# Kernel tuning notes

Hardware: AMD Instinct MI355X
Metric: run time of the kernel (lower is better)

Reference implementation:

```python
import jax, jax.numpy as jnp
import numpy as np

B, S, E = 8, 4096, 128

def _prelu(x, a):
    return jnp.where(x >= 0, x, a * x)

def setup_inputs() -> dict:
    key = jax.random.key(0)
    ks = jax.random.split(key, 7)
    lim = 1.0 / np.sqrt(E)
    x = jax.random.normal(ks[0], (B, S, E), dtype=jnp.float32)
    Wq = jax.random.uniform(ks[1], (E, E), jnp.float32, -lim, lim)
    Wk = jax.random.uniform(ks[2], (E, E), jnp.float32, -lim, lim)
    Wv = jax.random.uniform(ks[3], (E, E), jnp.float32, -lim, lim)
    bq = jax.random.uniform(ks[4], (E,), jnp.float32, -lim, lim)
    bk = jax.random.uniform(ks[5], (E,), jnp.float32, -lim, lim)
    bv = jax.random.uniform(ks[6], (E,), jnp.float32, -lim, lim)
    # PReLU default: single shared slope initialized to 0.25
    aq = jnp.array(0.25, dtype=jnp.float32)
    ak = jnp.array(0.25, dtype=jnp.float32)
    av = jnp.array(0.25, dtype=jnp.float32)
    return {"x": x, "Wq": Wq, "bq": bq, "aq": aq,
            "Wk": Wk, "bk": bk, "ak": ak,
            "Wv": Wv, "bv": bv, "av": av}

def reference(x, Wq, bq, aq, Wk, bk, ak, Wv, bv, av):
    # Linear (y = x @ W.T + b) followed by PReLU, per nn.Sequential(Linear, PReLU)
    qx = _prelu(jnp.einsum('bse,fe->bsf', x, Wq) + bq, aq)  # [B,S,E]
    kx = _prelu(jnp.einsum('bse,fe->bsf', x, Wk) + bk, ak)
    vx = _prelu(jnp.einsum('bse,fe->bsf', x, Wv) + bv, av)
    scale = 1.0 / jnp.sqrt(jnp.asarray(E, dtype=x.dtype))
    qk = jnp.einsum('bqe,bke->bqk', qx, kx) * scale  # [B,S,S]
    attn = jax.nn.softmax(qk, axis=2)
    return jnp.einsum('bqk,bke->bqe', attn, vx)  # [B,S,E]
```

## Files before the change

### kernel.cpp

```cpp
#include <hip/hip_runtime.h>
#include <hip/hip_bf16.h>
#include <stdint.h>

typedef __bf16 bf16x8 __attribute__((ext_vector_type(8)));
typedef float f32x4 __attribute__((ext_vector_type(4)));
typedef float f32x16 __attribute__((ext_vector_type(16)));
typedef unsigned int u32x4 __attribute__((ext_vector_type(4)));

static constexpr int Bn = 8, Sn = 4096, En = 128;

__device__ __forceinline__ unsigned short f2bf(float f) {
  unsigned u = __builtin_bit_cast(unsigned, f);
  u += 0x7fffu + ((u >> 16) & 1u);
  return (unsigned short)(u >> 16);
}

__device__ __forceinline__ float bf2f(unsigned short s) {
  return __builtin_bit_cast(float, (unsigned)s << 16);
}

__device__ __forceinline__ unsigned cvtpk(float a, float b) {
  unsigned r;
  asm("v_cvt_pk_bf16_f32 %0, %1, %2" : "=v"(r) : "v"(a), "v"(b));
  return r;
}

__device__ __forceinline__ void plswap(unsigned &a, unsigned &b) {
  asm("v_permlane32_swap_b32 %0, %1" : "+v"(a), "+v"(b));
}

__global__ __launch_bounds__(256) void wconv_kernel(
    const float* __restrict__ Wq, const float* __restrict__ Wk,
    const float* __restrict__ Wv, unsigned short* __restrict__ wb)
{
  const int f4 = blockIdx.x * 256 + threadIdx.x;
  const int mat = f4 >> 12, off = f4 & 4095;
  const float* src = (mat == 0) ? Wq : (mat == 1) ? Wk : Wv;
  const float4 v = *(const float4*)&src[off * 4];
  ushort4 pk;
  pk.x = f2bf(v.x); pk.y = f2bf(v.y); pk.z = f2bf(v.z); pk.w = f2bf(v.w);
  *(ushort4*)&wb[(size_t)mat * 16384 + off * 4] = pk;
}

__global__ __launch_bounds__(512) void qkv_kernel(
    const float* __restrict__ x, const unsigned short* __restrict__ wb,
    const float* __restrict__ bq, const float* __restrict__ aq,
    const float* __restrict__ bk, const float* __restrict__ ak,
    const float* __restrict__ bv, const float* __restrict__ av,
    unsigned short* __restrict__ qo, unsigned short* __restrict__ kf,
    unsigned short* __restrict__ vf)
{
  __shared__ __align__(16) unsigned short xs[128 * 136];
  __shared__ __align__(16) unsigned short wsh[128 * 136];
  const int tid = threadIdx.x;
  const int r0 = blockIdx.x * 128;

  for (int i = 0; i < 8; ++i) {
    int cid = tid + i * 512;
    int row = cid >> 5, c4 = cid & 31;
    const float4 v = *(const float4*)&x[(size_t)(r0 + row) * 128 + c4 * 4];
    unsigned short* d = &xs[row * 136 + c4 * 4];
    d[0] = f2bf(v.x); d[1] = f2bf(v.y); d[2] = f2bf(v.z); d[3] = f2bf(v.w);
  }

  const int lane = tid & 63, wid = tid >> 6;
  const int g = lane >> 4, ln = lane & 15;
  const float* Bs[3] = {bq, bk, bv};
  const float* As[3] = {aq, ak, av};
  bf16x8 afrag[4];

  for (int mat = 0; mat < 3; ++mat) {
    __syncthreads();
    for (int i = 0; i < 4; ++i) {
      int cid = tid + i * 512;
      int row = cid >> 4, c8 = cid & 15;
      *(uint4*)&wsh[row * 136 + c8 * 8] =
          *(const uint4*)&wb[(size_t)mat * 16384 + row * 128 + c8 * 8];
    }
    __syncthreads();

    if (mat == 0) {
      for (int ks = 0; ks < 4; ++ks)
        afrag[ks] = *(const bf16x8*)&xs[(wid * 16 + ln) * 136 + ks * 32 + g * 8];
    }
    const float alpha = As[mat][0];
    f32x4 acc[8];
    for (int nt = 0; nt < 8; ++nt) acc[nt] = (f32x4)(0.f);
    for (int nt = 0; nt < 8; ++nt)
      for (int ks = 0; ks < 4; ++ks) {
        bf16x8 bfrag = *(const bf16x8*)&wsh[(nt * 16 + ln) * 136 + ks * 32 + g * 8];
        acc[nt] = __builtin_amdgcn_mfma_f32_16x16x32_bf16(afrag[ks], bfrag, acc[nt], 0, 0, 0);
      }
    const int mbase = r0 + wid * 16 + g * 4;
    for (int nt = 0; nt < 8; ++nt) {
      const int n = nt * 16 + ln;
      const float bias = Bs[mat][n];
      float vv[4];
      for (int r = 0; r < 4; ++r) {
        float t = acc[nt][r] + bias;
        vv[r] = t >= 0.f ? t : alpha * t;
      }
      if (mat == 0) {
        for (int r = 0; r < 4; ++r) qo[(size_t)(mbase + r) * 128 + n] = f2bf(vv[r]);
      } else if (mat == 1) {
        for (int r = 0; r < 4; ++r) {
          const int key = mbase + r, bb = key >> 12, sl = key & 4095;
          const size_t addr = ((size_t)bb << 20) + (size_t)(sl >> 5) * 8192
                            + nt * 1024 + ((ln >> 3) & 1) * 512
                            + (sl & 31) * 16 + ((ln & 7) << 1);
          *(unsigned short*)((char*)kf + addr) = f2bf(vv[r]);
        }
      } else {
        const int bb = mbase >> 12, sl = mbase & 4095;
        const int kb64 = sl >> 6, kk = sl & 63;
        const int ks2 = kk >> 4, hi2 = (kk >> 3) & 1, j0 = kk & 7;
        const size_t addr = ((size_t)bb << 20) + (size_t)kb64 * 16384
                          + (n >> 5) * 4096 + ks2 * 1024 + hi2 * 512
                          + (n & 31) * 16 + (j0 << 1);
        ushort4 pk;
        pk.x = f2bf(vv[0]); pk.y = f2bf(vv[1]); pk.z = f2bf(vv[2]); pk.w = f2bf(vv[3]);
        *(ushort4*)((char*)vf + addr) = pk;
      }
    }
  }
}

__device__ __forceinline__ void load_frag(const char* kfb, const char* vfb, int kt,
                                          int tid, uint4* kr, uint4* vr) {
  const char* ks = kfb + (size_t)kt * 16384;
  const char* vs = vfb + (size_t)kt * 16384;
  kr[0] = *(const uint4*)(ks + tid * 16);
  kr[1] = *(const uint4*)(ks + 8192 + tid * 16);
  vr[0] = *(const uint4*)(vs + tid * 16);
  vr[1] = *(const uint4*)(vs + 8192 + tid * 16);
}

__device__ __forceinline__ void store_frag(char* slot, int tid,
                                           const uint4* kr, const uint4* vr) {
  *(uint4*)(slot + tid * 16) = kr[0];
  *(uint4*)(slot + 8192 + tid * 16) = kr[1];
  *(uint4*)(slot + 16384 + tid * 16) = vr[0];
  *(uint4*)(slot + 24576 + tid * 16) = vr[1];
}

template <int KSPLIT>
__global__ __launch_bounds__(512, 2) void attn_kernel(
    const unsigned short* __restrict__ q,
    const unsigned short* __restrict__ kf,
    const unsigned short* __restrict__ vf,
    unsigned short* __restrict__ opart, float* __restrict__ mpart,
    float* __restrict__ lpart, float* __restrict__ out)
{
  __shared__ __align__(16) char smem[98304];
  const int tid = threadIdx.x;
  const int lane = tid & 63, wid = tid >> 6;
  const int NS = 8 * KSPLIT;
  const int bid = blockIdx.x;
  const int s_ = bid % NS;
  const int qt = bid / NS;
  const int b  = s_ / KSPLIT;
  const int kh = s_ % KSPLIT;
  const int hi = lane >> 5, ln = lane & 31;
  const size_t bOff = (size_t)b * Sn * En;

  const int nkt = (Sn / KSPLIT) / 64;
  const int kbase = kh * (Sn / KSPLIT);
  const char* kfb = (const char*)kf + ((size_t)b << 20) + (size_t)(kbase >> 5) * 8192;
  const char* vfb = (const char*)vf + ((size_t)b << 20) + (size_t)(kbase >> 6) * 16384;

  const int qrow = qt * 256 + wid * 32 + ln;
  bf16x8 qf[8];
  #pragma unroll
  for (int s = 0; s < 8; ++s)
    qf[s] = *(const bf16x8*)((const char*)(q + bOff) + (size_t)qrow * 256 + s * 32 + hi * 16);

  f32x16 acc[4];
  #pragma unroll
  for (int et = 0; et < 4; ++et) acc[et] = (f32x16)(0.f);
  float m_run = -1e30f, lsum = 0.f;

  const float cst = 1.4426950408889634f * 0.08838834764831845f;

  auto qk = [&](const char* slot, f32x16& st0, f32x16& st1) {
    const char* kp = slot + hi * 512 + ln * 16;
    st0 = (f32x16)(0.f); st1 = (f32x16)(0.f);
    __builtin_amdgcn_s_setprio(1);
    #pragma unroll
    for (int s = 0; s < 8; ++s) {
      bf16x8 kf0 = *(const bf16x8*)(kp + s * 1024);
      bf16x8 kf1 = *(const bf16x8*)(kp + 8192 + s * 1024);
      st0 = __builtin_amdgcn_mfma_f32_32x32x16_bf16(kf0, qf[s], st0, 0, 0, 0);
      st1 = __builtin_amdgcn_mfma_f32_32x32x16_bf16(kf1, qf[s], st1, 0, 0, 0);
    }
    __builtin_amdgcn_s_setprio(0);
  };

  auto sm_pv = [&](const char* slot, const f32x16& st0, const f32x16& st1) {
    const char* vp = slot + 16384 + hi * 512 + ln * 16;
    float t16[16];
    #pragma unroll
    for (int i = 0; i < 16; ++i) t16[i] = fmaxf(st0[i], st1[i]);
    float t8[8];
    #pragma unroll
    for (int i = 0; i < 8; ++i) t8[i] = fmaxf(t16[i], t16[i + 8]);
    float t4[4];
    #pragma unroll
    for (int i = 0; i < 4; ++i) t4[i] = fmaxf(t8[i], t8[i + 4]);
    float vtile = fmaxf(fmaxf(t4[0], t4[1]), fmaxf(t4[2], t4[3])) * cst;
    vtile = fmaxf(vtile, __shfl_xor(vtile, 32));

    if (__any(vtile > m_run + 8.0f)) {
      float mnew = fmaxf(m_run, vtile);
      float al = __builtin_amdgcn_exp2f(m_run - mnew);
      #pragma unroll
      for (int et = 0; et < 4; ++et) acc[et] *= al;
      lsum *= al;
      m_run = mnew;
    }

    float p[32];
    #pragma unroll
    for (int i = 0; i < 16; ++i) p[i]      = __builtin_amdgcn_exp2f(fmaf(st0[i], cst, -m_run));
    #pragma unroll
    for (int i = 0; i < 16; ++i) p[16 + i] = __builtin_amdgcn_exp2f(fmaf(st1[i], cst, -m_run));

    float s16[16];
    #pragma unroll
    for (int i = 0; i < 16; ++i) s16[i] = p[i] + p[16 + i];
    float s8[8];
    #pragma unroll
    for (int i = 0; i < 8; ++i) s8[i] = s16[i] + s16[i + 8];
    float s4[4];
    #pragma unroll
    for (int i = 0; i < 4; ++i) s4[i] = s8[i] + s8[i + 4];
    float tsum = (s4[0] + s4[1]) + (s4[2] + s4[3]);
    tsum += __shfl_xor(tsum, 32);
    lsum += tsum;

    unsigned wa[8], wb2[8];
    #pragma unroll
    for (int g2 = 0; g2 < 8; ++g2) {
      wa[g2]  = cvtpk(p[4 * g2], p[4 * g2 + 1]);
      wb2[g2] = cvtpk(p[4 * g2 + 2], p[4 * g2 + 3]);
    }
    bf16x8 pb[4];
    #pragma unroll
    for (int ks = 0; ks < 4; ++ks) {
      unsigned w0 = wa[2 * ks], w2 = wa[2 * ks + 1];
      plswap(w0, w2);
      unsigned w1 = wb2[2 * ks], w3 = wb2[2 * ks + 1];
      plswap(w1, w3);
      u32x4 w = {w0, w1, w2, w3};
      pb[ks] = __builtin_bit_cast(bf16x8, w);
    }

    __builtin_amdgcn_s_setprio(1);
    #pragma unroll
    for (int ks = 0; ks < 4; ++ks) {
      #pragma unroll
      for (int et = 0; et < 4; ++et) {
        bf16x8 vfr = *(const bf16x8*)(vp + et * 4096 + ks * 1024);
        acc[et] = __builtin_amdgcn_mfma_f32_32x32x16_bf16(vfr, pb[ks], acc[et], 0, 0, 0);
      }
    }
    __builtin_amdgcn_s_setprio(0);
  };

  char* s0 = smem;
  char* s1 = smem + 32768;
  char* s2 = smem + 65536;

  uint4 kregA[2], vregA[2], kregB[2], vregB[2];
  load_frag(kfb, vfb, 0, tid, kregA, vregA);
  store_frag(s0, tid, kregA, vregA);
  load_frag(kfb, vfb, 1, tid, kregB, vregB);
  store_frag(s1, tid, kregB, vregB);
  if (nkt > 2) load_frag(kfb, vfb, 2, tid, kregA, vregA);
  __syncthreads();
  f32x16 sA0, sA1, sB0, sB1;
  qk(s0, sA0, sA1);

  for (int t = 0; t < nkt; t += 2) {
    if (t + 2 < nkt) store_frag(s2, tid, kregA, vregA);
    if (t + 3 < nkt) load_frag(kfb, vfb, t + 3, tid, kregB, vregB);
    qk(s1, sB0, sB1);
    sm_pv(s0, sA0, sA1);
    __syncthreads();

    if (t + 3 < nkt) store_frag(s0, tid, kregB, vregB);
    if (t + 4 < nkt) load_frag(kfb, vfb, t + 4, tid, kregA, vregA);
    if (t + 2 < nkt) qk(s2, sA0, sA1);
    sm_pv(s1, sB0, sB1);
    __syncthreads();

    char* tt = s0; s0 = s2; s2 = s1; s1 = tt;
  }

  if (KSPLIT > 1 && lane < 32) {
    const size_t idx = (size_t)kh * (Bn * Sn) + (size_t)b * Sn + qt * 256 + wid * 32 + ln;
    mpart[idx] = m_run;
    lpart[idx] = lsum;
  }

  __syncthreads();
  const float inv = (KSPLIT == 1) ? (1.0f / lsum) : 1.0f;
  char* sl = smem + wid * 8192;
  char* outb;
  if (KSPLIT == 1)
    outb = (char*)(out + ((size_t)b * Sn + qt * 256 + wid * 32) * En);
  else
    outb = (char*)(opart + ((size_t)kh * (Bn * Sn) + (size_t)b * Sn + qt * 256 + wid * 32) * En);

  #pragma unroll
  for (int h = 0; h < 2; ++h) {
    #pragma unroll
    for (int e2 = 0; e2 < 2; ++e2) {
      const int et = 2 * h + e2;
      #pragma unroll
      for (int rg = 0; rg < 4; ++rg) {
        f32x4 v;
        #pragma unroll
        for (int j = 0; j < 4; ++j) v[j] = acc[et][rg * 4 + j] * inv;
        const int addr = ln * 256 + e2 * 128 + rg * 32 + hi * 16;
        *(f32x4*)(sl + (addr ^ ((ln & 7) << 4))) = v;
      }
    }
    asm volatile("s_waitcnt lgkmcnt(0)" ::: "memory");
    __builtin_amdgcn_sched_barrier(0);
    #pragma unroll
    for (int i = 0; i < 8; ++i) {
      const int flat = i * 1024 + lane * 16;
      const int qr = flat >> 8, col = flat & 255;
      f32x4 v = *(const f32x4*)(sl + ((qr * 256 + col) ^ ((qr & 7) << 4)));
      if (KSPLIT == 1) {
        *(f32x4*)(outb + (size_t)qr * 512 + h * 256 + col) = v;
      } else {
        ushort4 pk;
        pk.x = f2bf(v[0]); pk.y = f2bf(v[1]); pk.z = f2bf(v[2]); pk.w = f2bf(v[3]);
        *(ushort4*)(outb + (size_t)qr * 256 + h * 128 + (col >> 1)) = pk;
      }
    }
    if (h == 0) {
      asm volatile("s_waitcnt lgkmcnt(0)" ::: "memory");
      __builtin_amdgcn_sched_barrier(0);
    }
  }
}

template <int NSPLIT>
__global__ __launch_bounds__(256) void combine_kernel(
    const unsigned short* __restrict__ op, const float* __restrict__ mp,
    const float* __restrict__ lp, float* __restrict__ out)
{
  const int idx = blockIdx.x * 256 + threadIdx.x;
  const int row = idx >> 5;
  const int BS = Bn * Sn;
  float m = -1e30f;
  #pragma unroll
  for (int j = 0; j < NSPLIT; ++j) m = fmaxf(m, mp[j * BS + row]);
  float den = 0.f;
  f32x4 sum = (f32x4)(0.f);
  #pragma unroll
  for (int j = 0; j < NSPLIT; ++j) {
    const float w = __builtin_amdgcn_exp2f(mp[j * BS + row] - m);
    den += w * lp[j * BS + row];
    ushort4 u = *(const ushort4*)(op + (size_t)j * ((size_t)BS * En) + (size_t)idx * 4);
    f32x4 o;
    o[0] = bf2f(u.x); o[1] = bf2f(u.y); o[2] = bf2f(u.z); o[3] = bf2f(u.w);
    sum += o * w;
  }
  const float inv = 1.f / den;
  ((f32x4*)out)[idx] = sum * inv;
}

extern "C" void kernel_launch(void* const* d_in, const int* in_sizes, int n_in,
                              void* d_out, int out_size, void* d_ws, size_t ws_size,
                              hipStream_t stream) {
  const float* x  = (const float*)d_in[0];
  const float* Wq = (const float*)d_in[1];
  const float* bq = (const float*)d_in[2];
  const float* aq = (const float*)d_in[3];
  const float* Wk = (const float*)d_in[4];
  const float* bk = (const float*)d_in[5];
  const float* ak = (const float*)d_in[6];
  const float* Wv = (const float*)d_in[7];
  const float* bv = (const float*)d_in[8];
  const float* av = (const float*)d_in[9];

  const size_t BSE = (size_t)Bn * Sn * En;
  const size_t BS  = (size_t)Bn * Sn;
  char* base = (char*)d_ws;
  unsigned short* qws = (unsigned short*)base;
  unsigned short* kws = qws + BSE;
  unsigned short* vws = kws + BSE;
  const size_t fixed = 3 * BSE * 2;
  unsigned short* opart = (unsigned short*)(base + fixed);

  auto need = [&](int j) {
    return fixed + (size_t)j * BSE * 2 + (size_t)j * BS * 8 + 98304;
  };
  int split = 1;
  if (ws_size >= need(2)) split = 2;

  float* mpart = (float*)(base + fixed + (size_t)split * BSE * 2);
  float* lpart = mpart + (size_t)split * BS;
  unsigned short* wb = (unsigned short*)(lpart + (size_t)split * BS);

  wconv_kernel<<<48, 256, 0, stream>>>(Wq, Wk, Wv, wb);
  qkv_kernel<<<256, 512, 0, stream>>>(x, wb, bq, aq, bk, ak, bv, av,
                                      qws, kws, vws);
  if (split == 2) {
    attn_kernel<2><<<256, 512, 0, stream>>>(qws, kws, vws, opart, mpart, lpart,
                                            (float*)d_out);
    combine_kernel<2><<<4096, 256, 0, stream>>>(opart, mpart, lpart, (float*)d_out);
  } else {
    attn_kernel<1><<<128, 512, 0, stream>>>(qws, kws, vws, opart, mpart, lpart,
                                            (float*)d_out);
  }
}
```

Baseline: 134.8 us.

## Add 4-way key-split attention kernel with XCC-aware ticket scheduling

Adds an attention kernel that splits the key dimension four ways and launches 512 blocks instead of 256, writing bf16 partial outputs plus per-row max and sum that a 4-way combine kernel merges. Each block claims a ticket through an atomic on a per-XCC counter, so the tiles sharing a batch's K/V are placed on the same XCD to improve L2 reuse. The aim is more parallelism and occupancy (launch bounds 512,4) on the mi355x. The cost is extra partial-output traffic, a memset, a heavier combine pass, and more workspace.

```diff
diff --git a/kernel.cpp b/kernel.cpp
--- a/kernel.cpp
+++ b/kernel.cpp
@@ -347,6 +347,197 @@
   }
 }
 
+__global__ __launch_bounds__(512, 4) void attn4_kernel(
+    const unsigned short* __restrict__ q,
+    const unsigned short* __restrict__ kf,
+    const unsigned short* __restrict__ vf,
+    unsigned short* __restrict__ opart, float* __restrict__ mpart,
+    float* __restrict__ lpart, unsigned* __restrict__ tickets)
+{
+  __shared__ __align__(16) char smem[65536];
+  __shared__ int tk_sh;
+  const int tid = threadIdx.x;
+  const int lane = tid & 63, wid = tid >> 6;
+  const int hi = lane >> 5, ln = lane & 31;
+
+  if (tid == 0) {
+    unsigned xcc;
+    asm volatile("s_getreg_b32 %0, hwreg(HW_REG_XCC_ID)" : "=s"(xcc));
+    xcc &= 7u;
+    int t = -1;
+    for (int i = 0; i < 8; ++i) {
+      unsigned qx2 = (xcc + (unsigned)i) & 7u;
+      unsigned old = atomicAdd(&tickets[qx2], 1u);
+      if (old < 64u) { t = (int)(qx2 * 64u + old); break; }
+    }
+    tk_sh = t;
+  }
+  __syncthreads();
+  const int tk = tk_sh;
+  const int qx = tk >> 6, idx = tk & 63;
+  const int s_ = qx + 8 * (idx & 3);
+  const int qt = idx >> 2;
+  const int b = s_ >> 2, kh = s_ & 3;
+
+  const size_t bOff = (size_t)b * Sn * En;
+  const int nkt = 16;
+  const int kbase = kh * 1024;
+  const char* kfb = (const char*)kf + ((size_t)b << 20) + (size_t)(kbase >> 5) * 8192;
+  const char* vfb = (const char*)vf + ((size_t)b << 20) + (size_t)(kbase >> 6) * 16384;
+
+  const int qrow = qt * 256 + wid * 32 + ln;
+  bf16x8 qf[8];
+  #pragma unroll
+  for (int s = 0; s < 8; ++s)
+    qf[s] = *(const bf16x8*)((const char*)(q + bOff) + (size_t)qrow * 256 + s * 32 + hi * 16);
+
+  f32x16 acc[4];
+  #pragma unroll
+  for (int et = 0; et < 4; ++et) acc[et] = (f32x16)(0.f);
+  float m_run = -1e30f, lsum = 0.f;
+  const float cst = 1.4426950408889634f * 0.08838834764831845f;
+
+  char* const s0 = smem;
+  char* const s1 = smem + 32768;
+
+  uint4 kreg[2], vreg[2];
+  load_frag(kfb, vfb, 0, tid, kreg, vreg);
+  store_frag(s0, tid, kreg, vreg);
+  load_frag(kfb, vfb, 1, tid, kreg, vreg);
+  __syncthreads();
+
+  for (int kt = 0; kt < nkt; ++kt) {
+    const char* cur = (kt & 1) ? s1 : s0;
+    const char* kp = cur + hi * 512 + ln * 16;
+    const char* vp = cur + 16384 + hi * 512 + ln * 16;
+
+    f32x16 st0 = (f32x16)(0.f), st1 = (f32x16)(0.f);
+    __builtin_amdgcn_s_setprio(1);
+    #pragma unroll
+    for (int s = 0; s < 8; ++s) {
+      bf16x8 kf0 = *(const bf16x8*)(kp + s * 1024);
+      bf16x8 kf1 = *(const bf16x8*)(kp + 8192 + s * 1024);
+      st0 = __builtin_amdgcn_mfma_f32_32x32x16_bf16(kf0, qf[s], st0, 0, 0, 0);
+      st1 = __builtin_amdgcn_mfma_f32_32x32x16_bf16(kf1, qf[s], st1, 0, 0, 0);
+    }
+    __builtin_amdgcn_s_setprio(0);
+
+    float t16[16];
+    #pragma unroll
+    for (int i = 0; i < 16; ++i) t16[i] = fmaxf(st0[i], st1[i]);
+    float t8[8];
+    #pragma unroll
+    for (int i = 0; i < 8; ++i) t8[i] = fmaxf(t16[i], t16[i + 8]);
+    float t4[4];
+    #pragma unroll
+    for (int i = 0; i < 4; ++i) t4[i] = fmaxf(t8[i], t8[i + 4]);
+    float vtile = fmaxf(fmaxf(t4[0], t4[1]), fmaxf(t4[2], t4[3])) * cst;
+    vtile = fmaxf(vtile, __shfl_xor(vtile, 32));
+
+    if (__any(vtile > m_run + 8.0f)) {
+      float mnew = fmaxf(m_run, vtile);
+      float al = __builtin_amdgcn_exp2f(m_run - mnew);
+      #pragma unroll
+      for (int et = 0; et < 4; ++et) acc[et] *= al;
+      lsum *= al;
+      m_run = mnew;
+    }
+
+    float p[32];
+    #pragma unroll
+    for (int i = 0; i < 16; ++i) p[i]      = __builtin_amdgcn_exp2f(fmaf(st0[i], cst, -m_run));
+    #pragma unroll
+    for (int i = 0; i < 16; ++i) p[16 + i] = __builtin_amdgcn_exp2f(fmaf(st1[i], cst, -m_run));
+
+    float s16[16];
+    #pragma unroll
+    for (int i = 0; i < 16; ++i) s16[i] = p[i] + p[16 + i];
+    float s8[8];
+    #pragma unroll
+    for (int i = 0; i < 8; ++i) s8[i] = s16[i] + s16[i + 8];
+    float s4[4];
+    #pragma unroll
+    for (int i = 0; i < 4; ++i) s4[i] = s8[i] + s8[i + 4];
+    float tsum = (s4[0] + s4[1]) + (s4[2] + s4[3]);
+    tsum += __shfl_xor(tsum, 32);
+    lsum += tsum;
+
+    unsigned wa[8], wb2[8];
+    #pragma unroll
+    for (int g2 = 0; g2 < 8; ++g2) {
+      wa[g2]  = cvtpk(p[4 * g2], p[4 * g2 + 1]);
+      wb2[g2] = cvtpk(p[4 * g2 + 2], p[4 * g2 + 3]);
+    }
+    bf16x8 pb[4];
+    #pragma unroll
+    for (int ks = 0; ks < 4; ++ks) {
+      unsigned w0 = wa[2 * ks], w2 = wa[2 * ks + 1];
+      plswap(w0, w2);
+      unsigned w1 = wb2[2 * ks], w3 = wb2[2 * ks + 1];
+      plswap(w1, w3);
+      u32x4 w = {w0, w1, w2, w3};
+      pb[ks] = __builtin_bit_cast(bf16x8, w);
+    }
+
+    __builtin_amdgcn_s_setprio(1);
+    #pragma unroll
+    for (int ks = 0; ks < 4; ++ks) {
+      #pragma unroll
+      for (int et = 0; et < 4; ++et) {
+        bf16x8 vfr = *(const bf16x8*)(vp + et * 4096 + ks * 1024);
+        acc[et] = __builtin_amdgcn_mfma_f32_32x32x16_bf16(vfr, pb[ks], acc[et], 0, 0, 0);
+      }
+    }
+    __builtin_amdgcn_s_setprio(0);
+
+    __syncthreads();
+    if (kt + 1 < nkt) store_frag((kt & 1) ? s0 : s1, tid, kreg, vreg);
+    __syncthreads();
+    if (kt + 2 < nkt) load_frag(kfb, vfb, kt + 2, tid, kreg, vreg);
+  }
+
+  if (lane < 32) {
+    const size_t idx2 = (size_t)kh * (Bn * Sn) + (size_t)b * Sn + qt * 256 + wid * 32 + ln;
+    mpart[idx2] = m_run;
+    lpart[idx2] = lsum;
+  }
+
+  __syncthreads();
+  char* sl = smem + wid * 8192;
+  char* outb = (char*)(opart + ((size_t)kh * (Bn * Sn) + (size_t)b * Sn + qt * 256 + wid * 32) * En);
+
+  #pragma unroll
+  for (int h = 0; h < 2; ++h) {
+    #pragma unroll
+    for (int e2 = 0; e2 < 2; ++e2) {
+      const int et = 2 * h + e2;
+      #pragma unroll
+      for (int rg = 0; rg < 4; ++rg) {
+        f32x4 v;
+        #pragma unroll
+        for (int j = 0; j < 4; ++j) v[j] = acc[et][rg * 4 + j];
+        const int addr = ln * 256 + e2 * 128 + rg * 32 + hi * 16;
+        *(f32x4*)(sl + (addr ^ ((ln & 7) << 4))) = v;
+      }
+    }
+    asm volatile("s_waitcnt lgkmcnt(0)" ::: "memory");
+    __builtin_amdgcn_sched_barrier(0);
+    #pragma unroll
+    for (int i = 0; i < 8; ++i) {
+      const int flat = i * 1024 + lane * 16;
+      const int qr = flat >> 8, col = flat & 255;
+      f32x4 v = *(const f32x4*)(sl + ((qr * 256 + col) ^ ((qr & 7) << 4)));
+      ushort4 pk;
+      pk.x = f2bf(v[0]); pk.y = f2bf(v[1]); pk.z = f2bf(v[2]); pk.w = f2bf(v[3]);
+      *(ushort4*)(outb + (size_t)qr * 256 + h * 128 + (col >> 1)) = pk;
+    }
+    if (h == 0) {
+      asm volatile("s_waitcnt lgkmcnt(0)" ::: "memory");
+      __builtin_amdgcn_sched_barrier(0);
+    }
+  }
+}
+
 template <int NSPLIT>
 __global__ __launch_bounds__(256) void combine_kernel(
     const unsigned short* __restrict__ op, const float* __restrict__ mp,
@@ -397,19 +588,26 @@
   unsigned short* opart = (unsigned short*)(base + fixed);
 
   auto need = [&](int j) {
-    return fixed + (size_t)j * BSE * 2 + (size_t)j * BS * 8 + 98304;
+    return fixed + (size_t)j * BSE * 2 + (size_t)j * BS * 8 + 98304 + 256;
   };
   int split = 1;
-  if (ws_size >= need(2)) split = 2;
+  if (ws_size >= need(4)) split = 4;
+  else if (ws_size >= need(2)) split = 2;
 
   float* mpart = (float*)(base + fixed + (size_t)split * BSE * 2);
   float* lpart = mpart + (size_t)split * BS;
   unsigned short* wb = (unsigned short*)(lpart + (size_t)split * BS);
+  unsigned* tickets = (unsigned*)((char*)wb + 98304);
 
   wconv_kernel<<<48, 256, 0, stream>>>(Wq, Wk, Wv, wb);
   qkv_kernel<<<256, 512, 0, stream>>>(x, wb, bq, aq, bk, ak, bv, av,
                                       qws, kws, vws);
-  if (split == 2) {
+  if (split == 4) {
+    hipMemsetAsync(tickets, 0, 32, stream);
+    attn4_kernel<<<512, 512, 0, stream>>>(qws, kws, vws, opart, mpart, lpart,
+                                          tickets);
+    combine_kernel<4><<<4096, 256, 0, stream>>>(opart, mpart, lpart, (float*)d_out);
+  } else if (split == 2) {
     attn_kernel<2><<<256, 512, 0, stream>>>(qws, kws, vws, opart, mpart, lpart,
                                             (float*)d_out);
     combine_kernel<2><<<4096, 256, 0, stream>>>(opart, mpart, lpart, (float*)d_out);
```

Result: slower. 207.1 us (+53.7%).
